# Kernel optimization log

Measured on AMD Instinct MI355X. Metric: run time of the kernel, lower is better.

## Reference

```python
import jax, jax.numpy as jnp
import numpy as np

N_NODES = 50000
N_EDGES = 800000
IN_CH = 128
HID = 64
HEADS = 2
OUT_CH = 3
N_GRAPHS = 64
NEG_SLOPE = 0.2


def _gatv2(x, src, dst, Wl, Wr, att, bias, heads, out_ch, concat, n_nodes):
    # GATv2Conv (PyG semantics, eval mode, self-loops already appended)
    xl = (x @ Wl).reshape(n_nodes, heads, out_ch)  # lin_l -> source messages
    xr = (x @ Wr).reshape(n_nodes, heads, out_ch)  # lin_r -> target side
    e = jax.nn.leaky_relu(xl[src] + xr[dst], NEG_SLOPE)          # [E, H, C]
    alpha = jnp.einsum('ehc,hc->eh', e, att)                     # [E, H]
    # segment softmax over incoming edges of each target node
    amax = jax.ops.segment_max(alpha, dst, num_segments=n_nodes)  # [N, H]
    ea = jnp.exp(alpha - amax[dst])
    denom = jax.ops.segment_sum(ea, dst, num_segments=n_nodes)
    alpha = ea / (denom[dst] + 1e-16)
    msg = xl[src] * alpha[..., None]                             # [E, H, C]
    out = jax.ops.segment_sum(msg, dst, num_segments=n_nodes)    # [N, H, C]
    out = out.reshape(n_nodes, heads * out_ch) if concat else out.mean(axis=1)
    return out + bias


def setup_inputs() -> dict:
    key = jax.random.key(0)
    ks = jax.random.split(key, 12)
    x = jax.random.normal(ks[0], (N_NODES, IN_CH), dtype=jnp.float32)
    edge_index = jax.random.randint(ks[1], (2, N_EDGES), 0, N_NODES, dtype=jnp.int64 if jax.config.jax_enable_x64 else jnp.int32)
    batch = jnp.sort(jax.random.randint(ks[2], (N_NODES,), 0, N_GRAPHS))
    s = 0.05
    params = {
        'W1l': jax.random.normal(ks[3], (IN_CH, HEADS * HID), dtype=jnp.float32) * s,
        'W1r': jax.random.normal(ks[4], (IN_CH, HEADS * HID), dtype=jnp.float32) * s,
        'att1': jax.random.normal(ks[5], (HEADS, HID), dtype=jnp.float32) * s,
        'b1': jnp.zeros((HEADS * HID,), dtype=jnp.float32),
        'W2l': jax.random.normal(ks[6], (HEADS * HID, OUT_CH), dtype=jnp.float32) * s,
        'W2r': jax.random.normal(ks[7], (HEADS * HID, OUT_CH), dtype=jnp.float32) * s,
        'att2': jax.random.normal(ks[8], (1, OUT_CH), dtype=jnp.float32) * s,
        'b2': jnp.zeros((OUT_CH,), dtype=jnp.float32),
        'Wr1': jax.random.normal(ks[9], (OUT_CH, 64), dtype=jnp.float32) * s,
        'br1': jnp.zeros((64,), dtype=jnp.float32),
        'Wr2': jax.random.normal(ks[10], (64, 3), dtype=jnp.float32) * s,
        'br2': jnp.zeros((3,), dtype=jnp.float32),
    }
    return {'x': x, 'edge_index': edge_index, 'batch': batch, **params}


def reference(x, edge_index, batch, W1l, W1r, att1, b1, W2l, W2r, att2, b2, Wr1, br1, Wr2, br2):
    n = x.shape[0]
    loops = jnp.arange(n, dtype=edge_index.dtype)
    src = jnp.concatenate([edge_index[0], loops])  # add_self_loops=True
    dst = jnp.concatenate([edge_index[1], loops])
    h = _gatv2(x, src, dst, W1l, W1r, att1, b1, HEADS, HID, True, n)
    h = jax.nn.elu(h)
    h = _gatv2(h, src, dst, W2l, W2r, att2, b2, 1, OUT_CH, False, n)
    # global_mean_pool over graphs
    sums = jax.ops.segment_sum(h, batch, num_segments=N_GRAPHS)
    cnt = jax.ops.segment_sum(jnp.ones((n,), h.dtype), batch, num_segments=N_GRAPHS)
    g = sums / jnp.maximum(cnt, 1.0)[:, None]
    g = jax.nn.relu(g @ Wr1 + br1)
    return g @ Wr2 + br2
```

## Files before the change

### kernel.cpp

```cpp
#include <hip/hip_runtime.h>


#define NGRAPH 64
#define LOG2E 1.4426950408889634f

typedef __attribute__((ext_vector_type(2))) _Float16 hf2;

#define DPP_ROR(C, x) \
  __int_as_float(__builtin_amdgcn_update_dpp(0, __float_as_int(x), (0x120 | C), 0xF, 0xF, false))
#define DPP_QUAD(C, x) \
  __int_as_float(__builtin_amdgcn_update_dpp(0, __float_as_int(x), (C), 0xF, 0xF, false))

__device__ __forceinline__ float rowsum16(float v) {
  v += DPP_ROR(8, v);
  v += DPP_ROR(4, v);
  v += DPP_ROR(2, v);
  v += DPP_ROR(1, v);
  return v;
}

__device__ __forceinline__ unsigned bf16rne(float f) {
  unsigned u = __float_as_uint(f);
  return (u + 0x7FFFu + ((u >> 16) & 1u)) >> 16;
}

__device__ __forceinline__ unsigned short f16u(float f) {
  union { _Float16 h; unsigned short u; } v;
  v.h = (_Float16)f;
  return v.u;
}

__device__ __forceinline__ hf2 as_hf2(unsigned u) {
  union { unsigned u; hf2 h; } v;
  v.u = u;
  return v.h;
}

typedef __attribute__((ext_vector_type(8))) short bf16x8;
typedef __attribute__((ext_vector_type(4))) float f32x4;

__global__ void k_deg(const int* __restrict__ ei, int E, int Et,
                      int* __restrict__ deg, int* __restrict__ rank) {
  int e = blockIdx.x * blockDim.x + threadIdx.x;
  if (e >= Et) return;
  int d = (e < E) ? ei[E + e] : (e - E);
  rank[e] = atomicAdd(&deg[d], 1);
}

__global__ __launch_bounds__(256) void k_scan_part(const int* __restrict__ deg,
                                                   int* __restrict__ bsum, int n) {
  __shared__ int sd[256];
  int t = threadIdx.x;
  int i = blockIdx.x * 1024 + t * 4;
  int s = 0;
  if (i + 4 <= n) {
    int4 d = *(const int4*)&deg[i];
    s = d.x + d.y + d.z + d.w;
  } else {
    for (int j = i; j < min(i + 4, n); ++j) s += deg[j];
  }
  sd[t] = s;
  __syncthreads();
  for (int off = 128; off; off >>= 1) {
    if (t < off) sd[t] += sd[t + off];
    __syncthreads();
  }
  if (t == 0) bsum[blockIdx.x] = sd[0];
}

__global__ __launch_bounds__(256) void k_scan_write(const int* __restrict__ deg,
                                                    const int* __restrict__ bsum,
                                                    int* __restrict__ row_ptr,
                                                    int n, int nb) {
  __shared__ int sd[256];
  __shared__ int boff;
  int t = threadIdx.x;
  if (t < 64) {
    int v = (t < nb && t < (int)blockIdx.x) ? bsum[t] : 0;
#pragma unroll
    for (int off = 32; off; off >>= 1) v += __shfl_xor(v, off);
    if (t == 0) boff = v;
  }
  int i = blockIdx.x * 1024 + t * 4;
  int4 d = make_int4(0, 0, 0, 0);
  bool full = (i + 4 <= n);
  if (full) d = *(const int4*)&deg[i];
  else {
    if (i + 0 < n) d.x = deg[i + 0];
    if (i + 1 < n) d.y = deg[i + 1];
    if (i + 2 < n) d.z = deg[i + 2];
    if (i + 3 < n) d.w = deg[i + 3];
  }
  int s = d.x + d.y + d.z + d.w;
  sd[t] = s;
  __syncthreads();
  for (int off = 1; off < 256; off <<= 1) {
    int v = (t >= off) ? sd[t - off] : 0;
    __syncthreads();
    sd[t] += v;
    __syncthreads();
  }
  int ex = sd[t] - s + boff;
  int4 r;
  r.x = ex;
  r.y = ex + d.x;
  r.z = r.y + d.y;
  r.w = r.z + d.z;
  if (full) {
    *(int4*)&row_ptr[i] = r;
    if (i + 4 == n) row_ptr[n] = r.w + d.w;
  } else if (i < n) {
    int run = ex;
    int vals[4] = {d.x, d.y, d.z, d.w};
    for (int j = 0; j < 4 && i + j < n; ++j) {
      row_ptr[i + j] = run;
      run += vals[j];
    }
    if (i <= n && i + 4 > n) row_ptr[n] = run;
  }
}

__global__ void k_fill(const int* __restrict__ ei, int E, int Et,
                       const int* __restrict__ row_ptr,
                       const int* __restrict__ rank,
                       int* __restrict__ csr_src) {
  int e = blockIdx.x * blockDim.x + threadIdx.x;
  if (e >= Et) return;
  int s, d;
  if (e < E) { s = ei[e]; d = ei[E + e]; }
  else       { s = e - E; d = s; }
  csr_src[row_ptr[d] + rank[e]] = s;
}

__global__ __launch_bounds__(256) void k_cvtw(const float* __restrict__ W1l,
                                              const float* __restrict__ W1r,
                                              unsigned short* __restrict__ whp,
                                              unsigned short* __restrict__ wlp) {
  int t = threadIdx.x;
  int kc = t >> 6;
  int l = t & 63;
  int lr = l & 15;
  int k0 = kc * 32 + ((l >> 4) << 3);
  int b = blockIdx.x;
  int col = b * 16 + lr;
  float f[8];
#pragma unroll
  for (int j = 0; j < 8; ++j)
    f[j] = (col < 128) ? W1l[(size_t)(k0 + j) * 128 + col]
                       : W1r[(size_t)(k0 + j) * 128 + (col - 128)];
  unsigned hv[8], lv[8];
#pragma unroll
  for (int j = 0; j < 8; ++j) {
    hv[j] = bf16rne(f[j]);
    float r = f[j] - __uint_as_float(hv[j] << 16);
    lv[j] = bf16rne(r);
  }
  uint4 ph, pl;
  ph.x = hv[0] | (hv[1] << 16); ph.y = hv[2] | (hv[3] << 16);
  ph.z = hv[4] | (hv[5] << 16); ph.w = hv[6] | (hv[7] << 16);
  pl.x = lv[0] | (lv[1] << 16); pl.y = lv[2] | (lv[3] << 16);
  pl.z = lv[4] | (lv[5] << 16); pl.w = lv[6] | (lv[7] << 16);
  size_t slot = (((size_t)b * 4 + kc) * 64 + l) * 8;
  *(uint4*)&whp[slot] = ph;
  *(uint4*)&wlp[slot] = pl;
}

__global__ __launch_bounds__(256) void k_gmfma(const float* __restrict__ x,
                                               const unsigned short* __restrict__ whp,
                                               const unsigned short* __restrict__ wlp,
                                               unsigned short* __restrict__ outl,
                                               unsigned short* __restrict__ outr, int n) {
  __shared__ __align__(16) unsigned short xh_lds[2 * 4 * 64 * 8];
  __shared__ __align__(16) unsigned short xl_lds[2 * 4 * 64 * 8];
  int t = threadIdx.x;
  int skc = t >> 6;
  int sl = t & 63;
  int slr = sl & 15;
  int sk0 = skc * 32 + ((sl >> 4) << 3);
  int r0 = blockIdx.x * 32;

#pragma unroll
  for (int rb = 0; rb < 2; ++rb) {
    int row = r0 + rb * 16 + slr;
    float f[8];
    if (row < n) {
      float4 a = *(const float4*)&x[(size_t)row * 128 + sk0];
      float4 c = *(const float4*)&x[(size_t)row * 128 + sk0 + 4];
      f[0] = a.x; f[1] = a.y; f[2] = a.z; f[3] = a.w;
      f[4] = c.x; f[5] = c.y; f[6] = c.z; f[7] = c.w;
    } else {
#pragma unroll
      for (int j = 0; j < 8; ++j) f[j] = 0.f;
    }
    unsigned hv[8], lv[8];
#pragma unroll
    for (int j = 0; j < 8; ++j) {
      hv[j] = bf16rne(f[j]);
      float r = f[j] - __uint_as_float(hv[j] << 16);
      lv[j] = bf16rne(r);
    }
    uint4 ph, pl;
    ph.x = hv[0] | (hv[1] << 16); ph.y = hv[2] | (hv[3] << 16);
    ph.z = hv[4] | (hv[5] << 16); ph.w = hv[6] | (hv[7] << 16);
    pl.x = lv[0] | (lv[1] << 16); pl.y = lv[2] | (lv[3] << 16);
    pl.z = lv[4] | (lv[5] << 16); pl.w = lv[6] | (lv[7] << 16);
    int slot = ((rb * 4 + skc) * 64 + sl) * 8;
    *(uint4*)&xh_lds[slot] = ph;
    *(uint4*)&xl_lds[slot] = pl;
  }
  __syncthreads();

  int w = t >> 6;
  int lane = t & 63;
  int lr = lane & 15;

  f32x4 acc[2][4] = {};

#pragma unroll
  for (int kc = 0; kc < 4; ++kc) {
    bf16x8 ah[2], al[2], bh[4], bl[4];
#pragma unroll
    for (int m = 0; m < 2; ++m) {
      int slot = ((m * 4 + kc) * 64 + lane) * 8;
      ah[m] = *(const bf16x8*)&xh_lds[slot];
      al[m] = *(const bf16x8*)&xl_lds[slot];
    }
#pragma unroll
    for (int f = 0; f < 4; ++f) {
      size_t slot = (((size_t)(w * 4 + f) * 4 + kc) * 64 + lane) * 8;
      bh[f] = *(const bf16x8*)&whp[slot];
      bl[f] = *(const bf16x8*)&wlp[slot];
    }
#pragma unroll
    for (int m = 0; m < 2; ++m)
#pragma unroll
      for (int f = 0; f < 4; ++f) {
        acc[m][f] = __builtin_amdgcn_mfma_f32_16x16x32_bf16(ah[m], bh[f], acc[m][f], 0, 0, 0);
        acc[m][f] = __builtin_amdgcn_mfma_f32_16x16x32_bf16(ah[m], bl[f], acc[m][f], 0, 0, 0);
        acc[m][f] = __builtin_amdgcn_mfma_f32_16x16x32_bf16(al[m], bh[f], acc[m][f], 0, 0, 0);
      }
  }

  int rbase = (lane >> 4) * 4;
  unsigned short* dst = (w < 2) ? outl : outr;
  int cb = (w & 1) * 64;
#pragma unroll
  for (int m = 0; m < 2; ++m)
#pragma unroll
    for (int f = 0; f < 4; ++f) {
      int col = cb + f * 16 + lr;
#pragma unroll
      for (int i = 0; i < 4; ++i) {
        int row = r0 + m * 16 + rbase + i;
        if (row < n)
          dst[(size_t)row * 128 + col] = f16u(acc[m][f][i]);
      }
    }
}

__global__ __launch_bounds__(256) void k_fused1(const unsigned short* __restrict__ xl,
                                                const unsigned short* __restrict__ xr,
                                                const int* __restrict__ row_ptr,
                                                const int* __restrict__ csr_src,
                                                const float* __restrict__ att1,
                                                const float* __restrict__ b1,
                                                const float* __restrict__ W2l,
                                                const float* __restrict__ W2r,
                                                float* __restrict__ xl2,
                                                float* __restrict__ xr2, int n) {
  int wid  = (blockIdx.x * 256 + threadIdx.x) >> 6;
  int lane = threadIdx.x & 63;
  int sub  = lane & 31;
  int node = min(wid * 2 + (lane >> 5), n - 1);
  int ch = sub * 4;
  const char* xlb = (const char*)xl;
  unsigned chb = (unsigned)sub * 8u;

  uint2 xrq = *(const uint2*)&xr[(size_t)node * 128 + ch];
  hf2 xr01 = as_hf2(xrq.x), xr23 = as_hf2(xrq.y);
  float4 atv = *(const float4*)&att1[ch];
  hf2 at01, at23;
  at01.x = (_Float16)(atv.x * LOG2E); at01.y = (_Float16)(atv.y * LOG2E);
  at23.x = (_Float16)(atv.z * LOG2E); at23.y = (_Float16)(atv.w * LOG2E);
  hf2 k02; k02.x = (_Float16)0.2f; k02.y = (_Float16)0.2f;

  int s0 = row_ptr[node];
  int deg = row_ptr[node + 1] - s0;
  int odeg = __shfl_xor(deg, 32);
  int maxdeg = max(deg, odeg);
  int dm1 = deg - 1;
  const int* sp = csr_src + s0;

  float m = -1e30f, l = 0.f;
  float4 acc = make_float4(0.f, 0.f, 0.f, 0.f);

#define EDGE(p, x0, x1, x2, x3, q)                                      \
    { hf2 v01 = as_hf2(q.x), v23 = as_hf2(q.y);                         \
      hf2 t01 = v01 + xr01, t23 = v23 + xr23;                           \
      hf2 l01 = __builtin_elementwise_max(t01, t01 * k02);              \
      hf2 l23 = __builtin_elementwise_max(t23, t23 * k02);              \
      p = __builtin_amdgcn_fdot2(l23, at23,                             \
            __builtin_amdgcn_fdot2(l01, at01, 0.f, false), false);      \
      x0 = (float)v01.x; x1 = (float)v01.y;                             \
      x2 = (float)v23.x; x3 = (float)v23.y; }

  uint2 q0, q1, q2, q3;
  {
    int sA = sp[0];
    int sB = sp[min(1, dm1)];
    int sC = sp[min(2, dm1)];
    int sD = sp[min(3, dm1)];
    q0 = *(const uint2*)(xlb + (((unsigned)sA << 8) + chb));
    q1 = *(const uint2*)(xlb + (((unsigned)sB << 8) + chb));
    q2 = *(const uint2*)(xlb + (((unsigned)sC << 8) + chb));
    q3 = *(const uint2*)(xlb + (((unsigned)sD << 8) + chb));
  }

  for (int e = 0; e < maxdeg; e += 4) {
    int en = e + 4;
    int sA = sp[min(en + 0, dm1)];
    int sB = sp[min(en + 1, dm1)];
    int sC = sp[min(en + 2, dm1)];
    int sD = sp[min(en + 3, dm1)];
    uint2 f0 = *(const uint2*)(xlb + (((unsigned)sA << 8) + chb));
    uint2 f1 = *(const uint2*)(xlb + (((unsigned)sB << 8) + chb));
    uint2 f2 = *(const uint2*)(xlb + (((unsigned)sC << 8) + chb));
    uint2 f3 = *(const uint2*)(xlb + (((unsigned)sD << 8) + chb));

    float pa, pb, pc, pd;
    float xa0, xa1, xa2, xa3, xb0, xb1, xb2, xb3;
    float xc0, xc1, xc2, xc3, xd0, xd1, xd2, xd3;
    EDGE(pa, xa0, xa1, xa2, xa3, q0)
    EDGE(pb, xb0, xb1, xb2, xb3, q1)
    EDGE(pc, xc0, xc1, xc2, xc3, q2)
    EDGE(pd, xd0, xd1, xd2, xd3, q3)
    pa = rowsum16(pa);
    pb = rowsum16(pb);
    pc = rowsum16(pc);
    pd = rowsum16(pd);
    pa = (e + 0 < deg) ? pa : -1e30f;
    pb = (e + 1 < deg) ? pb : -1e30f;
    pc = (e + 2 < deg) ? pc : -1e30f;
    pd = (e + 3 < deg) ? pd : -1e30f;
    float mn = fmaxf(m, fmaxf(fmaxf(pa, pb), fmaxf(pc, pd)));
    float sc = exp2f(m - mn);
    float wa = exp2f(pa - mn);
    float wb = exp2f(pb - mn);
    float wc = exp2f(pc - mn);
    float wd = exp2f(pd - mn);
    acc.x = fmaf(wd, xd0, fmaf(wc, xc0, fmaf(wb, xb0, fmaf(wa, xa0, acc.x * sc))));
    acc.y = fmaf(wd, xd1, fmaf(wc, xc1, fmaf(wb, xb1, fmaf(wa, xa1, acc.y * sc))));
    acc.z = fmaf(wd, xd2, fmaf(wc, xc2, fmaf(wb, xb2, fmaf(wa, xa2, acc.z * sc))));
    acc.w = fmaf(wd, xd3, fmaf(wc, xc3, fmaf(wb, xb3, fmaf(wa, xa3, acc.w * sc))));
    l = fmaf(l, sc, wa + wb + wc + wd);
    m = mn;

    q0 = f0; q1 = f1; q2 = f2; q3 = f3;
  }
#undef EDGE

  float inv = 1.f / (l + 1e-16f);
  float4 b1v = *(const float4*)&b1[ch];
  float4 h;
  h.x = acc.x * inv + b1v.x; h.x = h.x > 0.f ? h.x : expm1f(h.x);
  h.y = acc.y * inv + b1v.y; h.y = h.y > 0.f ? h.y : expm1f(h.y);
  h.z = acc.z * inv + b1v.z; h.z = h.z > 0.f ? h.z : expm1f(h.z);
  h.w = acc.w * inv + b1v.w; h.w = h.w > 0.f ? h.w : expm1f(h.w);

  float4 u0 = *(const float4*)&W2l[ch * 3 + 0];
  float4 u1 = *(const float4*)&W2l[ch * 3 + 4];
  float4 u2 = *(const float4*)&W2l[ch * 3 + 8];
  float al0 = fmaf(h.w, u2.y, fmaf(h.z, u1.z, fmaf(h.y, u0.w, h.x * u0.x)));
  float al1 = fmaf(h.w, u2.z, fmaf(h.z, u1.w, fmaf(h.y, u1.x, h.x * u0.y)));
  float al2 = fmaf(h.w, u2.w, fmaf(h.z, u2.x, fmaf(h.y, u1.y, h.x * u0.z)));
  float4 v0 = *(const float4*)&W2r[ch * 3 + 0];
  float4 v1 = *(const float4*)&W2r[ch * 3 + 4];
  float4 v2 = *(const float4*)&W2r[ch * 3 + 8];
  float ar0 = fmaf(h.w, v2.y, fmaf(h.z, v1.z, fmaf(h.y, v0.w, h.x * v0.x)));
  float ar1 = fmaf(h.w, v2.z, fmaf(h.z, v1.w, fmaf(h.y, v1.x, h.x * v0.y)));
  float ar2 = fmaf(h.w, v2.w, fmaf(h.z, v2.x, fmaf(h.y, v1.y, h.x * v0.z)));
#pragma unroll
  for (int off = 1; off < 32; off <<= 1) {
    al0 += __shfl_xor(al0, off); al1 += __shfl_xor(al1, off);
    al2 += __shfl_xor(al2, off); ar0 += __shfl_xor(ar0, off);
    ar1 += __shfl_xor(ar1, off); ar2 += __shfl_xor(ar2, off);
  }
  if (sub == 0 && wid * 2 + (lane >> 5) < n) {
    *(float4*)&xl2[node * 4] = make_float4(al0, al1, al2, 0.f);
    *(float4*)&xr2[node * 4] = make_float4(ar0, ar1, ar2, 0.f);
  }
}

__global__ __launch_bounds__(256) void k_fused2(const float* __restrict__ xl2,
                                                const float* __restrict__ xr2,
                                                const int* __restrict__ row_ptr,
                                                const int* __restrict__ csr_src,
                                                const float* __restrict__ att2,
                                                const float* __restrict__ b2,
                                                const int* __restrict__ batch,
                                                float* __restrict__ gsum,
                                                float* __restrict__ gcnt, int n) {
  __shared__ float ls[NGRAPH * 3];
  __shared__ float lc[NGRAPH];
  int t = threadIdx.x;
  for (int i = t; i < NGRAPH * 3; i += 256) ls[i] = 0.f;
  for (int i = t; i < NGRAPH; i += 256) lc[i] = 0.f;
  __syncthreads();

  int node = (blockIdx.x * 256 + t) >> 2;
  int lane = t & 3;
  if (node < n) {
    float4 xrv = *(const float4*)&xr2[node * 4];
    float c0 = att2[0] * LOG2E, c1 = att2[1] * LOG2E, c2 = att2[2] * LOG2E;
    int s0 = row_ptr[node], s1 = row_ptr[node + 1];
    float m = -1e30f, l = 0.f, a0 = 0.f, a1 = 0.f, a2 = 0.f;
    for (int slot = s0 + lane; slot < s1; slot += 4) {
      int s = csr_src[slot];
      float4 xlv = *(const float4*)&xl2[s * 4];
      float t0 = xlv.x + xrv.x; t0 = fmaxf(t0, 0.2f * t0);
      float t1 = xlv.y + xrv.y; t1 = fmaxf(t1, 0.2f * t1);
      float t2 = xlv.z + xrv.z; t2 = fmaxf(t2, 0.2f * t2);
      float p = fmaf(t2, c2, fmaf(t1, c1, t0 * c0));
      float mn = fmaxf(m, p);
      float sc = exp2f(m - mn);
      float w  = exp2f(p - mn);
      a0 = a0 * sc + w * xlv.x;
      a1 = a1 * sc + w * xlv.y;
      a2 = a2 * sc + w * xlv.z;
      l = l * sc + w;
      m = mn;
    }
#define MERGEQ(C)                                                       \
    {                                                                   \
      float m2 = DPP_QUAD(C, m);                                        \
      float l2 = DPP_QUAD(C, l);                                        \
      float b0 = DPP_QUAD(C, a0);                                       \
      float b1v = DPP_QUAD(C, a1);                                      \
      float b2v = DPP_QUAD(C, a2);                                      \
      float mn = fmaxf(m, m2);                                          \
      float sA = exp2f(m - mn);                                         \
      float sB = exp2f(m2 - mn);                                        \
      a0 = a0 * sA + b0 * sB;                                           \
      a1 = a1 * sA + b1v * sB;                                          \
      a2 = a2 * sA + b2v * sB;                                          \
      l = l * sA + l2 * sB;                                             \
      m = mn;                                                           \
    }
    MERGEQ(0x39) MERGEQ(0x4E)
#undef MERGEQ
    if (lane == 0) {
      float inv = 1.f / (l + 1e-16f);
      float o0 = a0 * inv + b2[0];
      float o1 = a1 * inv + b2[1];
      float o2 = a2 * inv + b2[2];
      int b = batch[node];
      atomicAdd(&ls[b * 3 + 0], o0);
      atomicAdd(&ls[b * 3 + 1], o1);
      atomicAdd(&ls[b * 3 + 2], o2);
      atomicAdd(&lc[b], 1.f);
    }
  }
  __syncthreads();
  for (int i = t; i < NGRAPH * 3; i += 256)
    if (ls[i] != 0.f) atomicAdd(&gsum[i], ls[i]);
  for (int i = t; i < NGRAPH; i += 256)
    if (lc[i] != 0.f) atomicAdd(&gcnt[i], lc[i]);
}

__global__ __launch_bounds__(64) void k_mlp(const float* __restrict__ gsum,
                                            const float* __restrict__ gcnt,
                                            const float* __restrict__ Wr1,
                                            const float* __restrict__ br1,
                                            const float* __restrict__ Wr2,
                                            const float* __restrict__ br2,
                                            float* __restrict__ out) {
  int t = threadIdx.x;
  if (t >= NGRAPH) return;
  float cnt = fmaxf(gcnt[t], 1.f);
  float g0 = gsum[t * 3 + 0] / cnt;
  float g1 = gsum[t * 3 + 1] / cnt;
  float g2 = gsum[t * 3 + 2] / cnt;
  float o0 = br2[0], o1 = br2[1], o2 = br2[2];
  for (int j = 0; j < 64; ++j) {
    float hj = g0 * Wr1[j] + g1 * Wr1[64 + j] + g2 * Wr1[128 + j] + br1[j];
    hj = fmaxf(hj, 0.f);
    o0 = fmaf(hj, Wr2[j * 3 + 0], o0);
    o1 = fmaf(hj, Wr2[j * 3 + 1], o1);
    o2 = fmaf(hj, Wr2[j * 3 + 2], o2);
  }
  out[t * 3 + 0] = o0;
  out[t * 3 + 1] = o1;
  out[t * 3 + 2] = o2;
}

extern "C" void kernel_launch(void* const* d_in, const int* in_sizes, int n_in,
                              void* d_out, int out_size, void* d_ws, size_t ws_size,
                              hipStream_t stream) {
  const float* x    = (const float*)d_in[0];
  const int*   ei   = (const int*)d_in[1];
  const int*   batch= (const int*)d_in[2];
  const float* W1l  = (const float*)d_in[3];
  const float* W1r  = (const float*)d_in[4];
  const float* att1 = (const float*)d_in[5];
  const float* b1   = (const float*)d_in[6];
  const float* W2l  = (const float*)d_in[7];
  const float* W2r  = (const float*)d_in[8];
  const float* att2 = (const float*)d_in[9];
  const float* b2   = (const float*)d_in[10];
  const float* Wr1  = (const float*)d_in[11];
  const float* br1  = (const float*)d_in[12];
  const float* Wr2  = (const float*)d_in[13];
  const float* br2  = (const float*)d_in[14];
  float* out = (float*)d_out;

  const int N  = in_sizes[0] / 128;
  const int E  = in_sizes[1] / 2;
  const int Et = E + N;
  const int NB = (N + 1023) / 1024;
  const int NB32 = (N + 31) / 32;

  char* p = (char*)d_ws;
  auto alloc = [&](size_t bytes) -> char* {
    char* r = p;
    p += (bytes + 255) & ~(size_t)255;
    return r;
  };
  unsigned short* xl1 = (unsigned short*)alloc((size_t)N * 128 * 2);
  unsigned short* xr1 = (unsigned short*)alloc((size_t)N * 128 * 2);
  int*      row_ptr= (int*)alloc((size_t)(N + 1) * 4);
  int*      csr_src= (int*)alloc((size_t)Et * 4);
  int*      rank   = (int*)alloc((size_t)Et * 4);
  int*      bsum   = (int*)alloc(64 * 4);
  char*     z0     = p;
  int*      deg    = (int*)alloc((size_t)N * 4);
  float*    gsum   = (float*)alloc(NGRAPH * 3 * 4);
  float*    gcnt   = (float*)alloc(NGRAPH * 4);
  size_t    zbytes = (size_t)(p - z0);
  float*    xl2    = (float*)alloc((size_t)N * 4 * 4);
  float*    xr2    = (float*)alloc((size_t)N * 4 * 4);
  unsigned short* whp = (unsigned short*)alloc((size_t)16 * 2048 * 2);
  unsigned short* wlp = (unsigned short*)alloc((size_t)16 * 2048 * 2);

  hipMemsetAsync(z0, 0, zbytes, stream);
  hipLaunchKernelGGL(k_deg, dim3((Et + 255) / 256), dim3(256), 0, stream,
                     ei, E, Et, deg, rank);
  hipLaunchKernelGGL(k_scan_part, dim3(NB), dim3(256), 0, stream, deg, bsum, N);
  hipLaunchKernelGGL(k_scan_write, dim3(NB), dim3(256), 0, stream,
                     deg, bsum, row_ptr, N, NB);
  hipLaunchKernelGGL(k_fill, dim3((Et + 255) / 256), dim3(256), 0, stream,
                     ei, E, Et, row_ptr, rank, csr_src);
  hipLaunchKernelGGL(k_cvtw, dim3(16), dim3(256), 0, stream,
                     W1l, W1r, whp, wlp);
  hipLaunchKernelGGL(k_gmfma, dim3(NB32), dim3(256), 0, stream,
                     x, whp, wlp, xl1, xr1, N);
  int waves1 = (N + 1) / 2;
  hipLaunchKernelGGL(k_fused1, dim3((waves1 * 64 + 255) / 256), dim3(256), 0, stream,
                     xl1, xr1, row_ptr, csr_src, att1, b1, W2l, W2r, xl2, xr2, N);
  hipLaunchKernelGGL(k_fused2, dim3((N * 4 + 255) / 256), dim3(256), 0, stream,
                     xl2, xr2, row_ptr, csr_src, att2, b2, batch, gsum, gcnt, N);
  hipLaunchKernelGGL(k_mlp, dim3(1), dim3(64), 0, stream,
                     gsum, gcnt, Wr1, br1, Wr2, br2, out);
}
```

Measured before the change: 237.2 us.

## Merge prep kernels into shared launches and split fused1 into two halves

The weight conversion is folded into the degree-count kernel as extra blocks, and the CSR fill is folded into the MFMA projection kernel as extra blocks. This cuts the launch count and lets independent work share one grid. The first GAT aggregation kernel is now launched twice over node ranges, which adds one launch back. The reason for that split is not clear; it may aim at cache locality or scheduling.

```diff
diff --git a/kernel.cpp b/kernel.cpp
--- a/kernel.cpp
+++ b/kernel.cpp
@@ -39,9 +39,45 @@
 typedef __attribute__((ext_vector_type(8))) short bf16x8;
 typedef __attribute__((ext_vector_type(4))) float f32x4;
 
-__global__ void k_deg(const int* __restrict__ ei, int E, int Et,
-                      int* __restrict__ deg, int* __restrict__ rank) {
-  int e = blockIdx.x * blockDim.x + threadIdx.x;
+__global__ __launch_bounds__(256) void k_prep(const int* __restrict__ ei, int E, int Et,
+                                              int* __restrict__ deg,
+                                              int* __restrict__ rank,
+                                              const float* __restrict__ W1l,
+                                              const float* __restrict__ W1r,
+                                              unsigned short* __restrict__ whp,
+                                              unsigned short* __restrict__ wlp,
+                                              int degb) {
+  if ((int)blockIdx.x >= degb) {
+    int t = threadIdx.x;
+    int kc = t >> 6;
+    int l = t & 63;
+    int lr = l & 15;
+    int k0 = kc * 32 + ((l >> 4) << 3);
+    int b = (int)blockIdx.x - degb;
+    int col = b * 16 + lr;
+    float f[8];
+#pragma unroll
+    for (int j = 0; j < 8; ++j)
+      f[j] = (col < 128) ? W1l[(size_t)(k0 + j) * 128 + col]
+                         : W1r[(size_t)(k0 + j) * 128 + (col - 128)];
+    unsigned hv[8], lv[8];
+#pragma unroll
+    for (int j = 0; j < 8; ++j) {
+      hv[j] = bf16rne(f[j]);
+      float r = f[j] - __uint_as_float(hv[j] << 16);
+      lv[j] = bf16rne(r);
+    }
+    uint4 ph, pl;
+    ph.x = hv[0] | (hv[1] << 16); ph.y = hv[2] | (hv[3] << 16);
+    ph.z = hv[4] | (hv[5] << 16); ph.w = hv[6] | (hv[7] << 16);
+    pl.x = lv[0] | (lv[1] << 16); pl.y = lv[2] | (lv[3] << 16);
+    pl.z = lv[4] | (lv[5] << 16); pl.w = lv[6] | (lv[7] << 16);
+    size_t slot = (((size_t)b * 4 + kc) * 64 + l) * 8;
+    *(uint4*)&whp[slot] = ph;
+    *(uint4*)&wlp[slot] = pl;
+    return;
+  }
+  int e = blockIdx.x * 256 + threadIdx.x;
   if (e >= Et) return;
   int d = (e < E) ? ei[E + e] : (e - E);
   rank[e] = atomicAdd(&deg[d], 1);
@@ -120,58 +156,27 @@
   }
 }
 
-__global__ void k_fill(const int* __restrict__ ei, int E, int Et,
-                       const int* __restrict__ row_ptr,
-                       const int* __restrict__ rank,
-                       int* __restrict__ csr_src) {
-  int e = blockIdx.x * blockDim.x + threadIdx.x;
-  if (e >= Et) return;
-  int s, d;
-  if (e < E) { s = ei[e]; d = ei[E + e]; }
-  else       { s = e - E; d = s; }
-  csr_src[row_ptr[d] + rank[e]] = s;
-}
-
-__global__ __launch_bounds__(256) void k_cvtw(const float* __restrict__ W1l,
-                                              const float* __restrict__ W1r,
-                                              unsigned short* __restrict__ whp,
-                                              unsigned short* __restrict__ wlp) {
-  int t = threadIdx.x;
-  int kc = t >> 6;
-  int l = t & 63;
-  int lr = l & 15;
-  int k0 = kc * 32 + ((l >> 4) << 3);
-  int b = blockIdx.x;
-  int col = b * 16 + lr;
-  float f[8];
-#pragma unroll
-  for (int j = 0; j < 8; ++j)
-    f[j] = (col < 128) ? W1l[(size_t)(k0 + j) * 128 + col]
-                       : W1r[(size_t)(k0 + j) * 128 + (col - 128)];
-  unsigned hv[8], lv[8];
-#pragma unroll
-  for (int j = 0; j < 8; ++j) {
-    hv[j] = bf16rne(f[j]);
-    float r = f[j] - __uint_as_float(hv[j] << 16);
-    lv[j] = bf16rne(r);
-  }
-  uint4 ph, pl;
-  ph.x = hv[0] | (hv[1] << 16); ph.y = hv[2] | (hv[3] << 16);
-  ph.z = hv[4] | (hv[5] << 16); ph.w = hv[6] | (hv[7] << 16);
-  pl.x = lv[0] | (lv[1] << 16); pl.y = lv[2] | (lv[3] << 16);
-  pl.z = lv[4] | (lv[5] << 16); pl.w = lv[6] | (lv[7] << 16);
-  size_t slot = (((size_t)b * 4 + kc) * 64 + l) * 8;
-  *(uint4*)&whp[slot] = ph;
-  *(uint4*)&wlp[slot] = pl;
-}
-
-__global__ __launch_bounds__(256) void k_gmfma(const float* __restrict__ x,
-                                               const unsigned short* __restrict__ whp,
-                                               const unsigned short* __restrict__ wlp,
-                                               unsigned short* __restrict__ outl,
-                                               unsigned short* __restrict__ outr, int n) {
+__global__ __launch_bounds__(256) void k_gmfill(const float* __restrict__ x,
+                                                const unsigned short* __restrict__ whp,
+                                                const unsigned short* __restrict__ wlp,
+                                                unsigned short* __restrict__ outl,
+                                                unsigned short* __restrict__ outr,
+                                                int n, int gmb,
+                                                const int* __restrict__ ei, int E, int Et,
+                                                const int* __restrict__ row_ptr,
+                                                const int* __restrict__ rank,
+                                                int* __restrict__ csr_src) {
   __shared__ __align__(16) unsigned short xh_lds[2 * 4 * 64 * 8];
   __shared__ __align__(16) unsigned short xl_lds[2 * 4 * 64 * 8];
+  if ((int)blockIdx.x >= gmb) {
+    int e = ((int)blockIdx.x - gmb) * 256 + threadIdx.x;
+    if (e >= Et) return;
+    int s, d;
+    if (e < E) { s = ei[e]; d = ei[E + e]; }
+    else       { s = e - E; d = s; }
+    csr_src[row_ptr[d] + rank[e]] = s;
+    return;
+  }
   int t = threadIdx.x;
   int skc = t >> 6;
   int sl = t & 63;
@@ -267,11 +272,13 @@
                                                 const float* __restrict__ W2l,
                                                 const float* __restrict__ W2r,
                                                 float* __restrict__ xl2,
-                                                float* __restrict__ xr2, int n) {
+                                                float* __restrict__ xr2,
+                                                int b0, int cnt) {
   int wid  = (blockIdx.x * 256 + threadIdx.x) >> 6;
   int lane = threadIdx.x & 63;
   int sub  = lane & 31;
-  int node = min(wid * 2 + (lane >> 5), n - 1);
+  int rel  = min(wid * 2 + (lane >> 5), cnt - 1);
+  int node = b0 + rel;
   int ch = sub * 4;
   const char* xlb = (const char*)xl;
   unsigned chb = (unsigned)sub * 8u;
@@ -385,7 +392,7 @@
     al2 += __shfl_xor(al2, off); ar0 += __shfl_xor(ar0, off);
     ar1 += __shfl_xor(ar1, off); ar2 += __shfl_xor(ar2, off);
   }
-  if (sub == 0 && wid * 2 + (lane >> 5) < n) {
+  if (sub == 0 && wid * 2 + (lane >> 5) < cnt) {
     *(float4*)&xl2[node * 4] = make_float4(al0, al1, al2, 0.f);
     *(float4*)&xr2[node * 4] = make_float4(ar0, ar1, ar2, 0.f);
   }
@@ -518,6 +525,7 @@
   const int Et = E + N;
   const int NB = (N + 1023) / 1024;
   const int NB32 = (N + 31) / 32;
+  const int DEGB = (Et + 255) / 256;
 
   char* p = (char*)d_ws;
   auto alloc = [&](size_t bytes) -> char* {
@@ -542,20 +550,23 @@
   unsigned short* wlp = (unsigned short*)alloc((size_t)16 * 2048 * 2);
 
   hipMemsetAsync(z0, 0, zbytes, stream);
-  hipLaunchKernelGGL(k_deg, dim3((Et + 255) / 256), dim3(256), 0, stream,
-                     ei, E, Et, deg, rank);
+  hipLaunchKernelGGL(k_prep, dim3(DEGB + 16), dim3(256), 0, stream,
+                     ei, E, Et, deg, rank, W1l, W1r, whp, wlp, DEGB);
   hipLaunchKernelGGL(k_scan_part, dim3(NB), dim3(256), 0, stream, deg, bsum, N);
   hipLaunchKernelGGL(k_scan_write, dim3(NB), dim3(256), 0, stream,
                      deg, bsum, row_ptr, N, NB);
-  hipLaunchKernelGGL(k_fill, dim3((Et + 255) / 256), dim3(256), 0, stream,
+  hipLaunchKernelGGL(k_gmfill, dim3(NB32 + DEGB), dim3(256), 0, stream,
+                     x, whp, wlp, xl1, xr1, N, NB32,
                      ei, E, Et, row_ptr, rank, csr_src);
-  hipLaunchKernelGGL(k_cvtw, dim3(16), dim3(256), 0, stream,
-                     W1l, W1r, whp, wlp);
-  hipLaunchKernelGGL(k_gmfma, dim3(NB32), dim3(256), 0, stream,
-                     x, whp, wlp, xl1, xr1, N);
-  int waves1 = (N + 1) / 2;
-  hipLaunchKernelGGL(k_fused1, dim3((waves1 * 64 + 255) / 256), dim3(256), 0, stream,
-                     xl1, xr1, row_ptr, csr_src, att1, b1, W2l, W2r, xl2, xr2, N);
+  int M = (N / 2) & ~1;
+  int cnt0 = M, cnt1 = N - M;
+  int wv0 = (cnt0 + 1) / 2, wv1 = (cnt1 + 1) / 2;
+  hipLaunchKernelGGL(k_fused1, dim3((wv0 * 64 + 255) / 256), dim3(256), 0, stream,
+                     xl1, xr1, row_ptr, csr_src, att1, b1, W2l, W2r, xl2, xr2,
+                     0, cnt0);
+  hipLaunchKernelGGL(k_fused1, dim3((wv1 * 64 + 255) / 256), dim3(256), 0, stream,
+                     xl1, xr1, row_ptr, csr_src, att1, b1, W2l, W2r, xl2, xr2,
+                     M, cnt1);
   hipLaunchKernelGGL(k_fused2, dim3((N * 4 + 255) / 256), dim3(256), 0, stream,
                      xl2, xr2, row_ptr, csr_src, att2, b2, batch, gsum, gcnt, N);
   hipLaunchKernelGGL(k_mlp, dim3(1), dim3(64), 0, stream,
```

Result: no change. 238.0 us (+0.3%).
